# Optimization experiments

Measured on AMD Instinct MI355X. Metric: run time of the kernel, lower is better.

The kernel has to match this reference:

```python
import jax, jax.numpy as jnp
import numpy as np

B, C, H, W = 4, 256, 64, 64
GROUPS = 32
EPS = 1e-5


def setup_inputs() -> dict:
    key = jax.random.key(0)
    ks = jax.random.split(key, 8)
    s = 1.0 / np.sqrt(C)
    return {
        "Hand": jax.random.normal(ks[0], (B, C, H, W), jnp.float32),
        "U": jax.random.normal(ks[1], (B, C, H, W), jnp.float32),
        "WH_w": jax.random.normal(ks[2], (C, C), jnp.float32) * s,
        "WH_b": jax.random.normal(ks[3], (C,), jnp.float32) * 0.01,
        "WU_w": jax.random.normal(ks[4], (C, C), jnp.float32) * s,
        "WU_b": jax.random.normal(ks[5], (C,), jnp.float32) * 0.01,
        "gn_w": jax.random.normal(ks[6], (C,), jnp.float32) * 0.1,
        "gn_b": jax.random.normal(ks[7], (C,), jnp.float32) * 0.1,
    }


def _group_norm(x, w, b):
    # x: [B, C, H, W], normalize within each of GROUPS channel groups over (C//G, H, W)
    b_, c_, h_, w_ = x.shape
    xg = x.reshape(b_, GROUPS, c_ // GROUPS, h_, w_)
    mean = jnp.mean(xg, axis=(2, 3, 4), keepdims=True)
    var = jnp.var(xg, axis=(2, 3, 4), keepdims=True)
    xn = ((xg - mean) * jax.lax.rsqrt(var + EPS)).reshape(b_, c_, h_, w_)
    return xn * w[None, :, None, None] + b[None, :, None, None]


def reference(Hand, U, WH_w, WH_b, WU_w, WU_b, gn_w, gn_b):
    b_, c_, h_, w_ = Hand.shape
    n = h_ * w_
    Hf = Hand.reshape(b_, c_, n)  # [B, C, N]
    Uf = U.reshape(b_, c_, n)     # [B, C, N]
    # 1x1 convs == per-pixel linear on channels
    q = jnp.einsum('oc,bcn->bon', WH_w, Hf) + WH_b[None, :, None]  # [B, C, N]
    k = jnp.einsum('oc,bcn->bon', WU_w, Uf) + WU_b[None, :, None]  # [B, C, N]
    # affinity: A[b, n, m] = sum_c q[b,c,n] * k[b,c,m]  (unscaled)
    A = jnp.einsum('bcn,bcm->bnm', q, k)  # [B, N, N]
    A = jax.nn.softmax(A, axis=-1)
    out = jnp.einsum('bnm,bcm->bcn', A, Uf).reshape(b_, c_, h_, w_)
    return _group_norm(out, gn_w, gn_b) + Hand
```

## Files before the change

### kernel.cpp

```cpp
#include <hip/hip_runtime.h>
#include <hip/hip_fp16.h>
#include <math.h>


typedef _Float16 v8h __attribute__((ext_vector_type(8)));
typedef float    v4f __attribute__((ext_vector_type(4)));

#define NB 4
#define NC 256
#define NS 4096
#define NG 32
#define GEPS 1e-5f
#define NSPLIT 3

#define ASYNC_BARRIER() asm volatile("s_waitcnt lgkmcnt(0)\n\ts_barrier" ::: "memory")

template <int CTRL>
__device__ __forceinline__ float dpp_rot(float x) {
    int r = __builtin_amdgcn_update_dpp(__float_as_int(x), __float_as_int(x),
                                        CTRL, 0xF, 0xF, false);
    return __int_as_float(r);
}
__device__ __forceinline__ float row_max16(float x) {
    x = fmaxf(x, dpp_rot<0x128>(x));
    x = fmaxf(x, dpp_rot<0x124>(x));
    x = fmaxf(x, dpp_rot<0x122>(x));
    x = fmaxf(x, dpp_rot<0x121>(x));
    return x;
}
__device__ __forceinline__ float row_sum16(float x) {
    x = x + dpp_rot<0x128>(x);
    x = x + dpp_rot<0x124>(x);
    x = x + dpp_rot<0x122>(x);
    x = x + dpp_rot<0x121>(x);
    return x;
}

__global__ __launch_bounds__(256) void k_convert(const float* __restrict__ U,
    const float* __restrict__ Wh, const float* __restrict__ Wu,
    _Float16* __restrict__ Uh, _Float16* __restrict__ Wh16, _Float16* __restrict__ Wu16)
{
    const int i = blockIdx.x * 256 + threadIdx.x;
    Uh[i] = (_Float16)U[i];
    if (i < NC * NC) {
        const int o = i >> 8, c = i & 255;
        const int idx = ((((o >> 4) * 8 + (c >> 5)) * 4 + ((c >> 3) & 3)) * 16
                         + (o & 15)) * 8 + (c & 7);
        Wh16[idx] = (_Float16)Wh[i];
        Wu16[idx] = (_Float16)Wu[i];
    }
}

__global__ __launch_bounds__(256) void k_qkgemm(const float* __restrict__ Hand,
    const float* __restrict__ U, const _Float16* __restrict__ Wh16,
    const _Float16* __restrict__ Wu16, const float* __restrict__ WHb,
    const float* __restrict__ WUb, _Float16* __restrict__ qT, _Float16* __restrict__ kTsw)
{
    const int nt = blockIdx.x, b = blockIdx.y, z = blockIdx.z;
    const float*    X    = z ? U    : Hand;
    const _Float16* W    = z ? Wu16 : Wh16;
    const float*    bias = z ? WUb  : WHb;

    const int tid = threadIdx.x, w = tid >> 6, lane = tid & 63;
    const int q4 = lane >> 4, l15 = lane & 15;
    const int n = nt * 64 + w * 16 + l15;

    const float* Xcol = X + (size_t)b * NC * NS + n;
    v8h A[8];
#pragma unroll
    for (int kc = 0; kc < 8; ++kc) {
        const int c0 = kc * 32 + q4 * 8;
        v8h a;
#pragma unroll
        for (int j = 0; j < 8; ++j) a[j] = (_Float16)Xcol[(size_t)(c0 + j) * NS];
        A[kc] = a;
    }

#pragma unroll 4
    for (int osub = 0; osub < 16; ++osub) {
        const int o = osub * 16 + l15;
        v4f acc = {0.f, 0.f, 0.f, 0.f};
#pragma unroll
        for (int kc = 0; kc < 8; ++kc) {
            const v8h bf = *(const v8h*)(W + ((size_t)(osub * 8 + kc) * 64 + lane) * 8);
            acc = __builtin_amdgcn_mfma_f32_16x16x32_f16(A[kc], bf, acc, 0, 0, 0);
        }
        const float bv = bias[o];
        if (z == 0) {
            _Float16* orow = qT + ((size_t)b * NS + nt * 64 + w * 16 + q4 * 4) * NC + o;
#pragma unroll
            for (int r = 0; r < 4; ++r) orow[(size_t)r * NC] = (_Float16)(acc[r] + bv);
        } else {
            _Float16* kb = kTsw + (size_t)b * 128 * 8192;
#pragma unroll
            for (int r = 0; r < 4; ++r) {
                const int m = nt * 64 + w * 16 + q4 * 4 + r;
                kb[(size_t)(m >> 5) * 8192 + (m & 31) * 256
                   + (((o >> 3) ^ (m & 7)) * 8) + (o & 7)] = (_Float16)(acc[r] + bv);
            }
        }
    }
}

__global__ __launch_bounds__(256, 3) void k_attn(const _Float16* __restrict__ qT,
    const _Float16* __restrict__ kTsw, const _Float16* __restrict__ Uh,
    _Float16* __restrict__ Ppart, float* __restrict__ mstat, float* __restrict__ lstat)
{
    const int b  = blockIdx.x;
    const int nt = blockIdx.y;
    const int s  = blockIdx.z;
    const int t0 = (s == 0) ? 0 : (s == 1 ? 43 : 86);
    const int t1 = (s == 2) ? 128 : t0 + 43;

    __shared__ __align__(16) _Float16 Klds[2][32 * 256];
    __shared__ __align__(16) _Float16 Plds[64 * 32];
    __shared__ __align__(16) float alphaS[64];

    const int tid = threadIdx.x, w = tid >> 6, lane = tid & 63;
    const int q4 = lane >> 4, l15 = lane & 15;

    const _Float16* kTb = kTsw + (size_t)b * 128 * 8192;
    const _Float16* Uhb = Uh + (size_t)b * NC * NS;

    {
        const _Float16* src = kTb + (size_t)t0 * 8192;
#pragma unroll
        for (int j = 0; j < 4; ++j) {
            const int ch = w * 4 + j;
            __builtin_amdgcn_global_load_lds(
                (const __attribute__((address_space(1))) void*)(src + ch * 512 + lane * 8),
                (__attribute__((address_space(3))) void*)(&Klds[t0 & 1][ch * 512]), 16, 0, 0);
        }
    }

    v8h Q[8];
    {
        const _Float16* qrow = qT + ((size_t)b * NS + nt * 64 + w * 16 + l15) * NC;
#pragma unroll
        for (int kc = 0; kc < 8; ++kc) Q[kc] = *(const v8h*)(qrow + kc * 32 + q4 * 8);
    }

    v4f O[4][4];
#pragma unroll
    for (int i = 0; i < 4; ++i)
#pragma unroll
        for (int j = 0; j < 4; ++j) O[i][j] = (v4f){0.f, 0.f, 0.f, 0.f};
    float mi[4] = {-INFINITY, -INFINITY, -INFINITY, -INFINITY};
    float li[4] = {0.f, 0.f, 0.f, 0.f};

    for (int t = t0; t < t1; ++t) {
        const int p = t & 1;
        const int m0 = t * 32;

        v8h Ur[4];
#pragma unroll
        for (int js = 0; js < 4; ++js)
            Ur[js] = *(const v8h*)(Uhb + (size_t)(w * 64 + js * 16 + l15) * NS + m0 + q4 * 8);
        asm volatile("" ::: "memory");

        {
            const int tn = (t + 1 < t1) ? t + 1 : t0;
            const _Float16* src = kTb + (size_t)tn * 8192;
#pragma unroll
            for (int j = 0; j < 4; ++j) {
                const int ch = w * 4 + j;
                __builtin_amdgcn_global_load_lds(
                    (const __attribute__((address_space(1))) void*)(src + ch * 512 + lane * 8),
                    (__attribute__((address_space(3))) void*)(&Klds[p ^ 1][ch * 512]), 16, 0, 0);
            }
        }

        asm volatile("s_waitcnt vmcnt(8)" ::: "memory");
        ASYNC_BARRIER();

        v4f sv[2];
        sv[0] = (v4f){0.f, 0.f, 0.f, 0.f};
        sv[1] = (v4f){0.f, 0.f, 0.f, 0.f};
#pragma unroll
        for (int kc = 0; kc < 8; ++kc) {
#pragma unroll
            for (int ms = 0; ms < 2; ++ms) {
                const v8h kf = *(const v8h*)(&Klds[p][(ms * 16 + l15) * 256
                                             + (((kc * 4 + q4) ^ (l15 & 7)) * 8)]);
                sv[ms] = __builtin_amdgcn_mfma_f32_16x16x32_f16(Q[kc], kf, sv[ms], 0, 0, 0);
            }
        }

        float al[4];
#pragma unroll
        for (int r = 0; r < 4; ++r) {
            const float tm = row_max16(fmaxf(sv[0][r], sv[1][r]));
            const float mn = fmaxf(mi[r], tm);
            al[r] = __expf(mi[r] - mn);
            mi[r] = mn;
            const float p0 = __expf(sv[0][r] - mn);
            const float p1 = __expf(sv[1][r] - mn);
            sv[0][r] = p0; sv[1][r] = p1;
            li[r] = li[r] * al[r] + p0 + p1;
        }
        if (l15 == 0) {
#pragma unroll
            for (int r = 0; r < 4; ++r) alphaS[w * 16 + q4 * 4 + r] = al[r];
        }
#pragma unroll
        for (int ms = 0; ms < 2; ++ms)
#pragma unroll
            for (int r = 0; r < 4; ++r) {
                const int row = w * 16 + q4 * 4 + r;
                const int col = ms * 16 + l15;
                Plds[row * 32 + (((col >> 3) ^ ((row >> 2) & 3)) * 8) + (col & 7)]
                    = (_Float16)sv[ms][r];
            }
        ASYNC_BARRIER();

#pragma unroll
        for (int is = 0; is < 4; ++is) {
            const float4 av = *(const float4*)&alphaS[is * 16 + q4 * 4];
            const v4f aa = {av.x, av.y, av.z, av.w};
#pragma unroll
            for (int js = 0; js < 4; ++js) O[is][js] *= aa;
        }
#pragma unroll
        for (int is = 0; is < 4; ++is) {
            const v8h Pf = *(const v8h*)(&Plds[(is * 16 + l15) * 32
                                         + ((q4 ^ ((l15 >> 2) & 3)) * 8)]);
#pragma unroll
            for (int js = 0; js < 4; ++js)
                O[is][js] = __builtin_amdgcn_mfma_f32_16x16x32_f16(Pf, Ur[js], O[is][js], 0, 0, 0);
        }
    }

    asm volatile("s_waitcnt vmcnt(0)" ::: "memory");

#pragma unroll
    for (int r = 0; r < 4; ++r) li[r] = row_sum16(li[r]);
    if (l15 == 0) {
#pragma unroll
        for (int r = 0; r < 4; ++r) {
            const int n = nt * 64 + w * 16 + q4 * 4 + r;
            mstat[(size_t)(s * NB + b) * NS + n] = mi[r];
            lstat[(size_t)(s * NB + b) * NS + n] = li[r];
        }
    }
#pragma unroll
    for (int is = 0; is < 4; ++is)
#pragma unroll
        for (int js = 0; js < 4; ++js)
#pragma unroll
            for (int r = 0; r < 4; ++r) {
                _Float16* dst = Ppart + ((size_t)(s * NB + b) * NS + nt * 64 + is * 16
                                         + q4 * 4 + r) * NC + w * 64 + js * 16 + l15;
                __builtin_nontemporal_store((_Float16)O[is][js][r], dst);
            }
}

__global__ __launch_bounds__(256) void k_merge(const _Float16* __restrict__ Pp,
    const float* __restrict__ mstat, const float* __restrict__ lstat,
    float* __restrict__ Opre, float* __restrict__ statacc)
{
    const int b = blockIdx.y, tid = threadIdx.x;
    const int n = blockIdx.x * 8 + (tid >> 5);
    const int c0 = (tid & 31) * 8;
    const size_t nb = (size_t)b * NS + n;
    const size_t SP = (size_t)NB * NS;
    const float m0 = mstat[nb], m1 = mstat[SP + nb], m2 = mstat[2 * SP + nb];
    const float l0 = lstat[nb], l1 = lstat[SP + nb], l2 = lstat[2 * SP + nb];
    const float M  = fmaxf(m0, fmaxf(m1, m2));
    const float e0 = __expf(m0 - M), e1 = __expf(m1 - M), e2 = __expf(m2 - M);
    const float inv = 1.f / (e0 * l0 + e1 * l1 + e2 * l2);
    const float w0 = e0 * inv, w1 = e1 * inv, w2 = e2 * inv;
    const size_t base = nb * NC + c0;
    const v8h p0 = *(const v8h*)(Pp + base);
    const v8h p1 = *(const v8h*)(Pp + SP * NC + base);
    const v8h p2 = *(const v8h*)(Pp + 2 * SP * NC + base);
    float v[8];
    float s1 = 0.f, s2 = 0.f;
#pragma unroll
    for (int j = 0; j < 8; ++j) {
        v[j] = w0 * (float)p0[j] + w1 * (float)p1[j] + w2 * (float)p2[j];
        s1 += v[j]; s2 += v[j] * v[j];
    }
    *(float4*)(Opre + base)     = make_float4(v[0], v[1], v[2], v[3]);
    *(float4*)(Opre + base + 4) = make_float4(v[4], v[5], v[6], v[7]);

    __shared__ float r1[256], r2[256];
    r1[tid] = s1; r2[tid] = s2;
    __syncthreads();
    if (tid < 32) {
        float a = 0.f, q = 0.f;
#pragma unroll
        for (int k = 0; k < 8; ++k) { a += r1[tid + 32 * k]; q += r2[tid + 32 * k]; }
        atomicAdd(&statacc[(b * NG + tid) * 2 + 0], a);
        atomicAdd(&statacc[(b * NG + tid) * 2 + 1], q);
    }
}

__global__ __launch_bounds__(256) void k_gnapply(const float* __restrict__ Opre,
    const float* __restrict__ Hand, const float* __restrict__ gnw,
    const float* __restrict__ gnb, const float* __restrict__ statacc,
    float* __restrict__ out)
{
    const int nt = blockIdx.x, ct = blockIdx.y, b = blockIdx.z;
    __shared__ float buf[64 * 65];
    const int tid = threadIdx.x;
    {
        const int nr = tid >> 4, c4 = (tid & 15) * 4;
#pragma unroll
        for (int k = 0; k < 4; ++k) {
            const int n = nr + 16 * k;
            const float4 v = *(const float4*)(Opre + ((size_t)b * NS + nt * 64 + n) * NC
                                              + ct * 64 + c4);
            buf[n * 65 + c4 + 0] = v.x; buf[n * 65 + c4 + 1] = v.y;
            buf[n * 65 + c4 + 2] = v.z; buf[n * 65 + c4 + 3] = v.w;
        }
    }
    __syncthreads();
    const int nw = tid & 63, c0 = tid >> 6;
#pragma unroll
    for (int k = 0; k < 16; ++k) {
        const int cl = c0 + 4 * k;
        const int c  = ct * 64 + cl;
        const int g  = c >> 3;
        const float s1   = statacc[(b * NG + g) * 2 + 0];
        const float s2   = statacc[(b * NG + g) * 2 + 1];
        const float mean = s1 * (1.f / 32768.f);
        const float var  = s2 * (1.f / 32768.f) - mean * mean;
        const float rstd = rsqrtf(var + GEPS);
        const size_t oidx = ((size_t)b * NC + c) * NS + nt * 64 + nw;
        out[oidx] = (buf[nw * 65 + cl] - mean) * rstd * gnw[c] + gnb[c] + Hand[oidx];
    }
}

extern "C" void kernel_launch(void* const* d_in, const int* in_sizes, int n_in,
                              void* d_out, int out_size, void* d_ws, size_t ws_size,
                              hipStream_t stream)
{
    const float* Hand = (const float*)d_in[0];
    const float* U    = (const float*)d_in[1];
    const float* WHw  = (const float*)d_in[2];
    const float* WHb  = (const float*)d_in[3];
    const float* WUw  = (const float*)d_in[4];
    const float* WUb  = (const float*)d_in[5];
    const float* gnw  = (const float*)d_in[6];
    const float* gnb  = (const float*)d_in[7];
    float* out = (float*)d_out;

    char* ws = (char*)d_ws;
    _Float16* qT     = (_Float16*)(ws);
    _Float16* kTsw   = (_Float16*)(ws + 8388608);
    _Float16* Uh     = (_Float16*)(ws + 16777216);
    _Float16* Wh16   = (_Float16*)(ws + 25165824);
    _Float16* Wu16   = (_Float16*)(ws + 25296896);
    float*    mstat  = (float*)(ws + 25427968);
    float*    lstat  = (float*)(ws + 25624576);
    float*    statacc= (float*)(ws + 25821184);
    _Float16* Ppart  = (_Float16*)(ws + 25823232);
    float*    Opre   = (float*)(ws);

    hipMemsetAsync(statacc, 0, NB * NG * 2 * sizeof(float), stream);
    k_convert<<<dim3((NB * NC * NS) / 256), 256, 0, stream>>>(U, WHw, WUw, Uh, Wh16, Wu16);
    k_qkgemm <<<dim3(64, NB, 2), 256, 0, stream>>>(Hand, U, Wh16, Wu16, WHb, WUb, qT, kTsw);
    k_attn   <<<dim3(NB, 64, NSPLIT), 256, 0, stream>>>(qT, kTsw, Uh, Ppart, mstat, lstat);
    k_merge  <<<dim3(NS / 8, NB), 256, 0, stream>>>(Ppart, mstat, lstat, Opre, statacc);
    k_gnapply<<<dim3(64, 4, NB), 256, 0, stream>>>(Opre, Hand, gnw, gnb, statacc, out);
}
```

Measured before the change: 276.8 us.

## Fuse U fp16 conversion into QK GEMM and pad LDS tiles instead of XOR swizzle

The fp32-to-fp16 conversion of U moves out of the standalone convert kernel and into the k projection GEMM, which already loads U columns, so one full pass over U is dropped. The K and P shared-memory tiles switch from XOR swizzling to padded row strides (272 and 40 halves), which removes the swizzle index arithmetic. The K layout in global memory is padded to match, which makes each tile transfer 17 chunks instead of 16 and changes the vmcnt wait count. The extra Uh stores are strided column writes, which may be poorly coalesced, and the padded strides may bring back LDS bank conflicts.

```diff
diff --git a/kernel.cpp b/kernel.cpp
--- a/kernel.cpp
+++ b/kernel.cpp
@@ -12,6 +12,9 @@
 #define NG 32
 #define GEPS 1e-5f
 #define NSPLIT 3
+#define KSTRIDE 272
+#define KTILE   8704
+#define PSTRIDE 40
 
 #define ASYNC_BARRIER() asm volatile("s_waitcnt lgkmcnt(0)\n\ts_barrier" ::: "memory")
 
@@ -36,25 +39,22 @@
     return x;
 }
 
-__global__ __launch_bounds__(256) void k_convert(const float* __restrict__ U,
-    const float* __restrict__ Wh, const float* __restrict__ Wu,
-    _Float16* __restrict__ Uh, _Float16* __restrict__ Wh16, _Float16* __restrict__ Wu16)
+__global__ __launch_bounds__(256) void k_convert(const float* __restrict__ Wh,
+    const float* __restrict__ Wu, _Float16* __restrict__ Wh16, _Float16* __restrict__ Wu16)
 {
     const int i = blockIdx.x * 256 + threadIdx.x;
-    Uh[i] = (_Float16)U[i];
-    if (i < NC * NC) {
-        const int o = i >> 8, c = i & 255;
-        const int idx = ((((o >> 4) * 8 + (c >> 5)) * 4 + ((c >> 3) & 3)) * 16
-                         + (o & 15)) * 8 + (c & 7);
-        Wh16[idx] = (_Float16)Wh[i];
-        Wu16[idx] = (_Float16)Wu[i];
-    }
+    const int o = i >> 8, c = i & 255;
+    const int idx = ((((o >> 4) * 8 + (c >> 5)) * 4 + ((c >> 3) & 3)) * 16
+                     + (o & 15)) * 8 + (c & 7);
+    Wh16[idx] = (_Float16)Wh[i];
+    Wu16[idx] = (_Float16)Wu[i];
 }
 
 __global__ __launch_bounds__(256) void k_qkgemm(const float* __restrict__ Hand,
     const float* __restrict__ U, const _Float16* __restrict__ Wh16,
     const _Float16* __restrict__ Wu16, const float* __restrict__ WHb,
-    const float* __restrict__ WUb, _Float16* __restrict__ qT, _Float16* __restrict__ kTsw)
+    const float* __restrict__ WUb, _Float16* __restrict__ qT,
+    _Float16* __restrict__ kTsw, _Float16* __restrict__ Uh)
 {
     const int nt = blockIdx.x, b = blockIdx.y, z = blockIdx.z;
     const float*    X    = z ? U    : Hand;
@@ -76,6 +76,16 @@
         A[kc] = a;
     }
 
+    if (z == 1) {
+        _Float16* ub = Uh + (size_t)b * NC * NS + n;
+#pragma unroll
+        for (int kc = 0; kc < 8; ++kc) {
+            const int c0 = kc * 32 + q4 * 8;
+#pragma unroll
+            for (int j = 0; j < 8; ++j) ub[(size_t)(c0 + j) * NS] = A[kc][j];
+        }
+    }
+
 #pragma unroll 4
     for (int osub = 0; osub < 16; ++osub) {
         const int o = osub * 16 + l15;
@@ -91,12 +101,11 @@
 #pragma unroll
             for (int r = 0; r < 4; ++r) orow[(size_t)r * NC] = (_Float16)(acc[r] + bv);
         } else {
-            _Float16* kb = kTsw + (size_t)b * 128 * 8192;
+            _Float16* kb = kTsw + (size_t)b * 128 * KTILE;
 #pragma unroll
             for (int r = 0; r < 4; ++r) {
                 const int m = nt * 64 + w * 16 + q4 * 4 + r;
-                kb[(size_t)(m >> 5) * 8192 + (m & 31) * 256
-                   + (((o >> 3) ^ (m & 7)) * 8) + (o & 7)] = (_Float16)(acc[r] + bv);
+                kb[(size_t)(m >> 5) * KTILE + (m & 31) * KSTRIDE + o] = (_Float16)(acc[r] + bv);
             }
         }
     }
@@ -112,21 +121,21 @@
     const int t0 = (s == 0) ? 0 : (s == 1 ? 43 : 86);
     const int t1 = (s == 2) ? 128 : t0 + 43;
 
-    __shared__ __align__(16) _Float16 Klds[2][32 * 256];
-    __shared__ __align__(16) _Float16 Plds[64 * 32];
+    __shared__ __align__(16) _Float16 Klds[2][KTILE];
+    __shared__ __align__(16) _Float16 Plds[64 * PSTRIDE];
     __shared__ __align__(16) float alphaS[64];
 
     const int tid = threadIdx.x, w = tid >> 6, lane = tid & 63;
     const int q4 = lane >> 4, l15 = lane & 15;
 
-    const _Float16* kTb = kTsw + (size_t)b * 128 * 8192;
+    const _Float16* kTb = kTsw + (size_t)b * 128 * KTILE;
     const _Float16* Uhb = Uh + (size_t)b * NC * NS;
 
     {
-        const _Float16* src = kTb + (size_t)t0 * 8192;
-#pragma unroll
-        for (int j = 0; j < 4; ++j) {
-            const int ch = w * 4 + j;
+        const _Float16* src = kTb + (size_t)t0 * KTILE;
+#pragma unroll
+        for (int j = 0; j < 5; ++j) {
+            const int ch = (w * 5 + j) % 17;
             __builtin_amdgcn_global_load_lds(
                 (const __attribute__((address_space(1))) void*)(src + ch * 512 + lane * 8),
                 (__attribute__((address_space(3))) void*)(&Klds[t0 & 1][ch * 512]), 16, 0, 0);
@@ -160,17 +169,17 @@
 
         {
             const int tn = (t + 1 < t1) ? t + 1 : t0;
-            const _Float16* src = kTb + (size_t)tn * 8192;
-#pragma unroll
-            for (int j = 0; j < 4; ++j) {
-                const int ch = w * 4 + j;
+            const _Float16* src = kTb + (size_t)tn * KTILE;
+#pragma unroll
+            for (int j = 0; j < 5; ++j) {
+                const int ch = (w * 5 + j) % 17;
                 __builtin_amdgcn_global_load_lds(
                     (const __attribute__((address_space(1))) void*)(src + ch * 512 + lane * 8),
                     (__attribute__((address_space(3))) void*)(&Klds[p ^ 1][ch * 512]), 16, 0, 0);
             }
         }
 
-        asm volatile("s_waitcnt vmcnt(8)" ::: "memory");
+        asm volatile("s_waitcnt vmcnt(9)" ::: "memory");
         ASYNC_BARRIER();
 
         v4f sv[2];
@@ -180,8 +189,8 @@
         for (int kc = 0; kc < 8; ++kc) {
 #pragma unroll
             for (int ms = 0; ms < 2; ++ms) {
-                const v8h kf = *(const v8h*)(&Klds[p][(ms * 16 + l15) * 256
-                                             + (((kc * 4 + q4) ^ (l15 & 7)) * 8)]);
+                const v8h kf = *(const v8h*)(&Klds[p][(ms * 16 + l15) * KSTRIDE
+                                             + (kc * 4 + q4) * 8]);
                 sv[ms] = __builtin_amdgcn_mfma_f32_16x16x32_f16(Q[kc], kf, sv[ms], 0, 0, 0);
             }
         }
@@ -207,9 +216,7 @@
 #pragma unroll
             for (int r = 0; r < 4; ++r) {
                 const int row = w * 16 + q4 * 4 + r;
-                const int col = ms * 16 + l15;
-                Plds[row * 32 + (((col >> 3) ^ ((row >> 2) & 3)) * 8) + (col & 7)]
-                    = (_Float16)sv[ms][r];
+                Plds[row * PSTRIDE + ms * 16 + l15] = (_Float16)sv[ms][r];
             }
         ASYNC_BARRIER();
 
@@ -222,8 +229,7 @@
         }
 #pragma unroll
         for (int is = 0; is < 4; ++is) {
-            const v8h Pf = *(const v8h*)(&Plds[(is * 16 + l15) * 32
-                                         + ((q4 ^ ((l15 >> 2) & 3)) * 8)]);
+            const v8h Pf = *(const v8h*)(&Plds[(is * 16 + l15) * PSTRIDE + q4 * 8]);
 #pragma unroll
             for (int js = 0; js < 4; ++js)
                 O[is][js] = __builtin_amdgcn_mfma_f32_16x16x32_f16(Pf, Ur[js], O[is][js], 0, 0, 0);
@@ -348,18 +354,18 @@
     char* ws = (char*)d_ws;
     _Float16* qT     = (_Float16*)(ws);
     _Float16* kTsw   = (_Float16*)(ws + 8388608);
-    _Float16* Uh     = (_Float16*)(ws + 16777216);
-    _Float16* Wh16   = (_Float16*)(ws + 25165824);
-    _Float16* Wu16   = (_Float16*)(ws + 25296896);
-    float*    mstat  = (float*)(ws + 25427968);
-    float*    lstat  = (float*)(ws + 25624576);
-    float*    statacc= (float*)(ws + 25821184);
-    _Float16* Ppart  = (_Float16*)(ws + 25823232);
+    _Float16* Uh     = (_Float16*)(ws + 17301504);
+    _Float16* Wh16   = (_Float16*)(ws + 25690112);
+    _Float16* Wu16   = (_Float16*)(ws + 25821184);
+    float*    mstat  = (float*)(ws + 25952256);
+    float*    lstat  = (float*)(ws + 26148864);
+    float*    statacc= (float*)(ws + 26345472);
+    _Float16* Ppart  = (_Float16*)(ws + 26347520);
     float*    Opre   = (float*)(ws);
 
     hipMemsetAsync(statacc, 0, NB * NG * 2 * sizeof(float), stream);
-    k_convert<<<dim3((NB * NC * NS) / 256), 256, 0, stream>>>(U, WHw, WUw, Uh, Wh16, Wu16);
-    k_qkgemm <<<dim3(64, NB, 2), 256, 0, stream>>>(Hand, U, Wh16, Wu16, WHb, WUb, qT, kTsw);
+    k_convert<<<dim3((NC * NC) / 256), 256, 0, stream>>>(WHw, WUw, Wh16, Wu16);
+    k_qkgemm <<<dim3(64, NB, 2), 256, 0, stream>>>(Hand, U, Wh16, Wu16, WHb, WUb, qT, kTsw, Uh);
     k_attn   <<<dim3(NB, 64, NSPLIT), 256, 0, stream>>>(qT, kTsw, Uh, Ppart, mstat, lstat);
     k_merge  <<<dim3(NS / 8, NB), 256, 0, stream>>>(Ppart, mstat, lstat, Opre, statacc);
     k_gnapply<<<dim3(64, 4, NB), 256, 0, stream>>>(Opre, Hand, gnw, gnb, statacc, out);
```

After: 276.1 us. No clear change (-0.2%).
